# Kernel tuning notes

Measured on AMD Instinct MI355X. Metric: run time of the kernel, lower is better.

## Reference

```python
import math
import jax, jax.numpy as jnp
import numpy as np

B, S, D, H, FF = 2, 2048, 1024, 16, 4096
DH = D // H
NUM_BUCKETS, MAX_DISTANCE = 32, 128
EPS_LN = 1e-5


def setup_inputs() -> dict:
    key = jax.random.key(0)
    ks = jax.random.split(key, 12)
    sc = 0.02
    return {
        "x": jax.random.normal(ks[0], (B, S, D), dtype=jnp.float32),
        "Wq": jax.random.normal(ks[1], (D, D), dtype=jnp.float32) * sc,
        "bq": jnp.zeros((D,), jnp.float32),
        "Wk": jax.random.normal(ks[2], (D, D), dtype=jnp.float32) * sc,
        "bk": jnp.zeros((D,), jnp.float32),
        "Wv": jax.random.normal(ks[3], (D, D), dtype=jnp.float32) * sc,
        "bv": jnp.zeros((D,), jnp.float32),
        "Wo": jax.random.normal(ks[4], (D, D), dtype=jnp.float32) * sc,
        "bo": jnp.zeros((D,), jnp.float32),
        "W1": jax.random.normal(ks[5], (D, FF), dtype=jnp.float32) * sc,
        "b1": jnp.zeros((FF,), jnp.float32),
        "W2": jax.random.normal(ks[6], (FF, D), dtype=jnp.float32) * sc,
        "b2": jnp.zeros((D,), jnp.float32),
        "g1": jnp.ones((D,), jnp.float32),
        "beta1": jnp.zeros((D,), jnp.float32),
        "g2": jnp.ones((D,), jnp.float32),
        "beta2": jnp.zeros((D,), jnp.float32),
        "rel_emb": jax.random.normal(ks[7], (NUM_BUCKETS, H), dtype=jnp.float32) * sc,
        "pad_mask": jnp.ones((B, 1, 1, S), dtype=jnp.bool_),
    }


def _rel_bias(rel_emb, qlen, klen):
    # T5 bidirectional relative position bucketing; n = q_pos - k_pos
    q = jnp.arange(qlen)[:, None]
    k = jnp.arange(klen)[None, :]
    n = q - k
    half = NUM_BUCKETS // 2           # 16
    ret = (n < 0).astype(jnp.int32) * half
    n_abs = jnp.abs(n)
    max_exact = half // 2             # 8
    log_ratio = math.log(MAX_DISTANCE / max_exact)
    val_large = (max_exact + jnp.log(n_abs.astype(jnp.float32) / max_exact + 1e-6)
                 / log_ratio * (half - max_exact)).astype(jnp.int32)
    val_large = jnp.minimum(val_large, half - 1)
    bucket = jnp.where(n_abs < max_exact, n_abs.astype(jnp.int32), val_large) + ret
    bias = rel_emb[bucket]            # [Q, K, H]
    return jnp.transpose(bias, (2, 0, 1))[None]  # [1, H, Q, K]


def _layernorm(x, g, b):
    mu = jnp.mean(x, axis=-1, keepdims=True)
    var = jnp.mean(jnp.square(x - mu), axis=-1, keepdims=True)
    return (x - mu) * jax.lax.rsqrt(var + EPS_LN) * g + b


def reference(x, Wq, bq, Wk, bk, Wv, bv, Wo, bo, W1, b1, W2, b2,
              g1, beta1, g2, beta2, rel_emb, pad_mask):
    b_, s_, d_ = x.shape
    rel = _rel_bias(rel_emb, s_, s_)
    h = _layernorm(x, g1, beta1)
    q = (h @ Wq + bq).reshape(b_, s_, H, DH)
    k = (h @ Wk + bk).reshape(b_, s_, H, DH)
    v = (h @ Wv + bv).reshape(b_, s_, H, DH)
    scores = jnp.einsum("bqhd,bkhd->bhqk", q, k) / math.sqrt(DH)
    scores = scores + rel
    scores = jnp.where(pad_mask, scores, jnp.finfo(scores.dtype).min)
    attn = jax.nn.softmax(scores, axis=-1)
    out = jnp.einsum("bhqk,bkhd->bqhd", attn, v).reshape(b_, s_, d_)
    x = x + (out @ Wo + bo)
    h2 = _layernorm(x, g2, beta2)
    ff = jax.nn.gelu(h2 @ W1 + b1, approximate=False) @ W2 + b2
    return x + ff
```

## Files before the change

### kernel.cpp

```cpp
#include <hip/hip_runtime.h>
#include <hip/hip_bf16.h>
#include <math.h>

#define S_LEN 2048
#define DMODEL 1024
#define NHEAD 16
#define FFDIM 4096
#define NTOK 4096
#define QKV_LD 3072

typedef __attribute__((ext_vector_type(8))) short bf16x8;
typedef __attribute__((ext_vector_type(4))) float f32x4;

static __device__ __forceinline__ unsigned short f2bf_bits(float f) {
    union { __hip_bfloat16 b; unsigned short u; } cv;
    cv.b = __float2bfloat16(f);
    return cv.u;
}

__global__ __launch_bounds__(256) void transpose_bf16(
    const float* __restrict__ in, __hip_bfloat16* __restrict__ out, int R, int C)
{
    __shared__ float tile[32][33];
    const int c0 = blockIdx.x * 32, r0 = blockIdx.y * 32;
    const int tx = threadIdx.x & 31, ty = threadIdx.x >> 5;
#pragma unroll
    for (int i = 0; i < 4; i++) {
        int r = ty + i * 8;
        tile[r][tx] = in[(long)(r0 + r) * C + c0 + tx];
    }
    __syncthreads();
#pragma unroll
    for (int i = 0; i < 4; i++) {
        int c = ty + i * 8;
        out[(long)(c0 + c) * R + r0 + tx] = __float2bfloat16(tile[tx][c]);
    }
}

__global__ __launch_bounds__(256) void transpose_qkv_v(
    const __hip_bfloat16* __restrict__ in,
    __hip_bfloat16* __restrict__ out)
{
    __shared__ __hip_bfloat16 tile[32][33];
    const int bz = blockIdx.z;
    const int c0 = blockIdx.x * 32, r0 = blockIdx.y * 32;
    const int tx = threadIdx.x & 31, ty = threadIdx.x >> 5;
    const long ibase = (long)bz * S_LEN * QKV_LD;
#pragma unroll
    for (int i = 0; i < 4; i++) {
        int r = ty + i * 8;
        tile[r][tx] = in[ibase + (long)(r0 + r) * QKV_LD + c0 + tx];
    }
    __syncthreads();
    const long obase = (long)bz * DMODEL * S_LEN;
#pragma unroll
    for (int i = 0; i < 4; i++) {
        int c = ty + i * 8;
        out[obase + (long)(c0 + c) * S_LEN + r0 + tx] = tile[tx][c];
    }
}

__global__ __launch_bounds__(256) void biastab_kernel(
    const float* __restrict__ rel_emb, float* __restrict__ tab)
{
    int i = blockIdx.x * 256 + threadIdx.x;
    int h = i >> 12, idx = i & 4095;
    if (h >= NHEAD || idx >= 4095) return;
    int n = idx - 2047;
    int ret = (n < 0) ? 16 : 0;
    int na = (n < 0) ? -n : n;
    int bucket;
    if (na < 8) {
        bucket = na;
    } else {
        float vv = 8.0f + logf((float)na * 0.125f + 1e-6f) * (8.0f / 2.7725887222397811f);
        int vi = (int)vv;
        bucket = (vi < 15) ? vi : 15;
    }
    bucket += ret;
    tab[h * 4096 + idx] = rel_emb[bucket * NHEAD + h];
}

__global__ __launch_bounds__(256) void ln_bf16(
    const float* __restrict__ x, const float* __restrict__ gm,
    const float* __restrict__ bt, __hip_bfloat16* __restrict__ out)
{
    const long row = blockIdx.x;
    const int tid = threadIdx.x, w = tid >> 6;
    float4 v = ((const float4*)(x + row * DMODEL))[tid];
    float s = v.x + v.y + v.z + v.w;
#pragma unroll
    for (int m = 32; m >= 1; m >>= 1) s += __shfl_xor(s, m);
    __shared__ float red[4], red2[4];
    if ((tid & 63) == 0) red[w] = s;
    __syncthreads();
    float mu = (red[0] + red[1] + red[2] + red[3]) * (1.0f / DMODEL);
    float dx = v.x - mu, dy = v.y - mu, dz = v.z - mu, dw = v.w - mu;
    float s2 = dx * dx + dy * dy + dz * dz + dw * dw;
#pragma unroll
    for (int m = 32; m >= 1; m >>= 1) s2 += __shfl_xor(s2, m);
    if ((tid & 63) == 0) red2[w] = s2;
    __syncthreads();
    float var = (red2[0] + red2[1] + red2[2] + red2[3]) * (1.0f / DMODEL);
    float rs = rsqrtf(var + 1e-5f);
    float4 g4 = ((const float4*)gm)[tid];
    float4 b4 = ((const float4*)bt)[tid];
    long o = row * DMODEL + tid * 4;
    out[o + 0] = __float2bfloat16(dx * rs * g4.x + b4.x);
    out[o + 1] = __float2bfloat16(dy * rs * g4.y + b4.y);
    out[o + 2] = __float2bfloat16(dz * rs * g4.z + b4.z);
    out[o + 3] = __float2bfloat16(dw * rs * g4.w + b4.w);
}

template<int EPI>
__global__ __launch_bounds__(256) void gemm_bt(
    const __hip_bfloat16* __restrict__ A,
    const __hip_bfloat16* __restrict__ Bt,
    const float* __restrict__ bias,
    const float* __restrict__ bias2,
    const float* __restrict__ bias3,
    const float* __restrict__ resid,
    float* __restrict__ outf,
    __hip_bfloat16* __restrict__ outb,
    int K, int N)
{
    __shared__ __hip_bfloat16 As[128 * 32];
    __shared__ __hip_bfloat16 Bs[128 * 32];
    const int tid = threadIdx.x;
    const int lane = tid & 63, w = tid >> 6;
    const int cl = lane & 15, g = lane >> 4;
    const int wr = w >> 1, wc = w & 1;
    const int bm = blockIdx.x, bn = blockIdx.y;

    f32x4 acc[4][4] = {};

    const __hip_bfloat16* agp0 = A + (long)(bm * 128 + (tid >> 2)) * K + (tid & 3) * 8;
    const __hip_bfloat16* agp1 = agp0 + (long)64 * K;
    const __hip_bfloat16* bgp0 = Bt + (long)(bn * 128 + (tid >> 2)) * K + (tid & 3) * 8;
    const __hip_bfloat16* bgp1 = bgp0 + (long)64 * K;
    char* ldsA0 = (char*)As + w * 1024;
    char* ldsA1 = (char*)As + 4096 + w * 1024;
    char* ldsB0 = (char*)Bs + w * 1024;
    char* ldsB1 = (char*)Bs + 4096 + w * 1024;

    for (int k0 = 0; k0 < K; k0 += 32) {
        __syncthreads();
        __builtin_amdgcn_global_load_lds((const __attribute__((address_space(1))) void*)(agp0 + k0),
                                         (__attribute__((address_space(3))) void*)ldsA0, 16, 0, 0);
        __builtin_amdgcn_global_load_lds((const __attribute__((address_space(1))) void*)(agp1 + k0),
                                         (__attribute__((address_space(3))) void*)ldsA1, 16, 0, 0);
        __builtin_amdgcn_global_load_lds((const __attribute__((address_space(1))) void*)(bgp0 + k0),
                                         (__attribute__((address_space(3))) void*)ldsB0, 16, 0, 0);
        __builtin_amdgcn_global_load_lds((const __attribute__((address_space(1))) void*)(bgp1 + k0),
                                         (__attribute__((address_space(3))) void*)ldsB1, 16, 0, 0);
        __syncthreads();
        bf16x8 af[4], bfv[4];
#pragma unroll
        for (int m = 0; m < 4; m++)
            af[m] = *reinterpret_cast<const bf16x8*>(&As[(wr * 64 + m * 16 + cl) * 32 + g * 8]);
#pragma unroll
        for (int n = 0; n < 4; n++)
            bfv[n] = *reinterpret_cast<const bf16x8*>(&Bs[(wc * 64 + n * 16 + cl) * 32 + g * 8]);
#pragma unroll
        for (int m = 0; m < 4; m++)
#pragma unroll
            for (int n = 0; n < 4; n++)
                acc[m][n] = __builtin_amdgcn_mfma_f32_16x16x32_bf16(af[m], bfv[n], acc[m][n], 0, 0, 0);
    }

#pragma unroll
    for (int m = 0; m < 4; m++) {
#pragma unroll
        for (int n = 0; n < 4; n++) {
#pragma unroll
            for (int r = 0; r < 4; r++) {
                int row = bm * 128 + wr * 64 + m * 16 + g * 4 + r;
                int col = bn * 128 + wc * 64 + n * 16 + cl;
                long off = (long)row * N + col;
                if (EPI == 1) {
                    float vv = acc[m][n][r] + bias[col];
                    outf[off] = vv + resid[off];
                } else if (EPI == 2) {
                    float vv = acc[m][n][r] + bias[col];
                    float ge = 0.5f * vv * (1.0f + erff(vv * 0.70710678118654752f));
                    outb[off] = __float2bfloat16(ge);
                } else {
                    const float* bp = (col < 1024) ? bias : ((col < 2048) ? bias2 : bias3);
                    float vv = acc[m][n][r] + bp[col & 1023];
                    outb[off] = __float2bfloat16(vv);
                }
            }
        }
    }
}

__global__ __launch_bounds__(512, 4) void attn_fwd(
    const __hip_bfloat16* __restrict__ qkv,
    const __hip_bfloat16* __restrict__ vt,
    const float* __restrict__ btab,
    __hip_bfloat16* __restrict__ out)
{
    __shared__ __hip_bfloat16 Ks[2][64 * 64];
    __shared__ __hip_bfloat16 Vs[2][64 * 64];
    __shared__ __hip_bfloat16 Pl[8][16 * 64];
    const int tid = threadIdx.x, lane = tid & 63, w = tid >> 6;
    const int cl = lane & 15, g = lane >> 4;
    const int swz = (blockIdx.x & 7) * 64 + (blockIdx.x >> 3);
    const int bh = swz >> 4, qblk = swz & 15;
    const int b = bh >> 4, h = bh & 15;
    const int q0 = qblk * 128;
    const long qbase = ((long)b * S_LEN) * QKV_LD + h * 64;
    const __hip_bfloat16* vbase = vt + (long)b * DMODEL * S_LEN + (long)(h * 64) * S_LEN;

    const int srow = tid >> 3, scol = (tid & 7) ^ (srow & 7);
    const __hip_bfloat16* kstage = qkv + qbase + 1024 + (long)srow * QKV_LD + scol * 8;
    const __hip_bfloat16* vstage = vbase + (long)srow * S_LEN + scol * 8;

    const int qrow_a = q0 + w * 16 + cl;
    bf16x8 aq[2];
    aq[0] = *reinterpret_cast<const bf16x8*>(qkv + qbase + (long)qrow_a * QKV_LD + g * 8);
    aq[1] = *reinterpret_cast<const bf16x8*>(qkv + qbase + (long)qrow_a * QKV_LD + 32 + g * 8);

    f32x4 accO[4] = {};
    float mrun[4], lrun[4];
#pragma unroll
    for (int r = 0; r < 4; r++) { mrun[r] = -INFINITY; lrun[r] = 0.0f; }

    const int qrow_c = q0 + w * 16 + g * 4;

    auto STAGE = [&](int buf, int kv) {
        __builtin_amdgcn_global_load_lds(
            (const __attribute__((address_space(1))) void*)(kstage + (long)kv * QKV_LD),
            (__attribute__((address_space(3))) void*)((char*)&Ks[buf][0] + w * 1024), 16, 0, 0);
        __builtin_amdgcn_global_load_lds(
            (const __attribute__((address_space(1))) void*)(vstage + kv),
            (__attribute__((address_space(3))) void*)((char*)&Vs[buf][0] + w * 1024), 16, 0, 0);
    };

    STAGE(0, 0);
    __syncthreads();
    int cur = 0;

    for (int kv0 = 0; kv0 < S_LEN; kv0 += 64) {
        if (kv0 + 64 < S_LEN) STAGE(cur ^ 1, kv0 + 64);
        f32x4 accS[4] = {};
#pragma unroll
        for (int nf = 0; nf < 4; nf++) {
            int row = nf * 16 + cl;
#pragma unroll
            for (int ks2 = 0; ks2 < 2; ks2++) {
                int bo = row * 128 + ((((ks2 * 4 + g)) ^ (row & 7)) << 4);
                bf16x8 bk = *reinterpret_cast<const bf16x8*>((const char*)&Ks[cur][0] + bo);
                accS[nf] = __builtin_amdgcn_mfma_f32_16x16x32_bf16(aq[ks2], bk, accS[nf], 0, 0, 0);
            }
        }
        float sc[4][4], pmax[4];
#pragma unroll
        for (int r = 0; r < 4; r++) pmax[r] = -INFINITY;
#pragma unroll
        for (int nf = 0; nf < 4; nf++) {
            int col = kv0 + nf * 16 + cl;
#pragma unroll
            for (int r = 0; r < 4; r++) {
                int row = qrow_c + r;
                float s = accS[nf][r] * 0.125f + btab[h * 4096 + (row - col + 2047)];
                sc[nf][r] = s;
                pmax[r] = fmaxf(pmax[r], s);
            }
        }
#pragma unroll
        for (int r = 0; r < 4; r++) {
            pmax[r] = fmaxf(pmax[r], __shfl_xor(pmax[r], 1));
            pmax[r] = fmaxf(pmax[r], __shfl_xor(pmax[r], 2));
            pmax[r] = fmaxf(pmax[r], __shfl_xor(pmax[r], 4));
            pmax[r] = fmaxf(pmax[r], __shfl_xor(pmax[r], 8));
        }
        float mnew[4], alpha[4], psum[4];
#pragma unroll
        for (int r = 0; r < 4; r++) {
            mnew[r] = fmaxf(mrun[r], pmax[r]);
            alpha[r] = __expf(mrun[r] - mnew[r]);
            psum[r] = 0.0f;
        }
#pragma unroll
        for (int nf = 0; nf < 4; nf++) {
#pragma unroll
            for (int r = 0; r < 4; r++) {
                float p = __expf(sc[nf][r] - mnew[r]);
                psum[r] += p;
                int row_l = g * 4 + r, col_l = nf * 16 + cl;
                int bo = ((row_l * 64 + col_l) * 2) ^ ((row_l & 7) << 4);
                *reinterpret_cast<unsigned short*>(reinterpret_cast<char*>(&Pl[w][0]) + bo) = f2bf_bits(p);
            }
        }
#pragma unroll
        for (int r = 0; r < 4; r++) {
            psum[r] += __shfl_xor(psum[r], 1);
            psum[r] += __shfl_xor(psum[r], 2);
            psum[r] += __shfl_xor(psum[r], 4);
            psum[r] += __shfl_xor(psum[r], 8);
            lrun[r] = lrun[r] * alpha[r] + psum[r];
            mrun[r] = mnew[r];
#pragma unroll
            for (int df = 0; df < 4; df++) accO[df][r] *= alpha[r];
        }
        asm volatile("s_waitcnt lgkmcnt(0)" ::: "memory");
        __builtin_amdgcn_sched_barrier(0);
#pragma unroll
        for (int ks2 = 0; ks2 < 2; ks2++) {
            int bo = ((cl * 64 + ks2 * 32 + g * 8) * 2) ^ ((cl & 7) << 4);
            bf16x8 ap = *reinterpret_cast<const bf16x8*>(reinterpret_cast<const char*>(&Pl[w][0]) + bo);
#pragma unroll
            for (int df = 0; df < 4; df++) {
                int row = df * 16 + cl;
                int bo2 = row * 128 + ((((ks2 * 4 + g)) ^ (row & 7)) << 4);
                bf16x8 bv = *reinterpret_cast<const bf16x8*>((const char*)&Vs[cur][0] + bo2);
                accO[df] = __builtin_amdgcn_mfma_f32_16x16x32_bf16(ap, bv, accO[df], 0, 0, 0);
            }
        }
        __syncthreads();
        cur ^= 1;
    }
#pragma unroll
    for (int df = 0; df < 4; df++) {
#pragma unroll
        for (int r = 0; r < 4; r++) {
            int row = qrow_c + r;
            int col = df * 16 + cl;
            out[((long)b * S_LEN + row) * DMODEL + h * 64 + col] = __float2bfloat16(accO[df][r] / lrun[r]);
        }
    }
}

extern "C" void kernel_launch(void* const* d_in, const int* in_sizes, int n_in,
                              void* d_out, int out_size, void* d_ws, size_t ws_size,
                              hipStream_t stream) {
    (void)in_sizes; (void)n_in; (void)out_size; (void)ws_size;
    const float* x   = (const float*)d_in[0];
    const float* Wq  = (const float*)d_in[1];
    const float* bq  = (const float*)d_in[2];
    const float* Wk  = (const float*)d_in[3];
    const float* bk  = (const float*)d_in[4];
    const float* Wv  = (const float*)d_in[5];
    const float* bv  = (const float*)d_in[6];
    const float* Wo  = (const float*)d_in[7];
    const float* bo  = (const float*)d_in[8];
    const float* W1  = (const float*)d_in[9];
    const float* b1  = (const float*)d_in[10];
    const float* W2  = (const float*)d_in[11];
    const float* b2  = (const float*)d_in[12];
    const float* g1  = (const float*)d_in[13];
    const float* be1 = (const float*)d_in[14];
    const float* g2  = (const float*)d_in[15];
    const float* be2 = (const float*)d_in[16];
    const float* rel = (const float*)d_in[17];
    float* outp = (float*)d_out;

    char* ws = (char*)d_ws;
    __hip_bfloat16* Wqkvt = (__hip_bfloat16*)(ws + ((size_t)0  << 20));
    __hip_bfloat16* Wot   = (__hip_bfloat16*)(ws + ((size_t)6  << 20));
    __hip_bfloat16* W1t   = (__hip_bfloat16*)(ws + ((size_t)8  << 20));
    __hip_bfloat16* W2t   = (__hip_bfloat16*)(ws + ((size_t)16 << 20));
    __hip_bfloat16* hb    = (__hip_bfloat16*)(ws + ((size_t)24 << 20));
    __hip_bfloat16* qkvb  = (__hip_bfloat16*)(ws + ((size_t)32 << 20));
    __hip_bfloat16* vtb   = (__hip_bfloat16*)(ws + ((size_t)56 << 20));
    __hip_bfloat16* ao    = (__hip_bfloat16*)(ws + ((size_t)64 << 20));
    float*          x2    = (float*)         (ws + ((size_t)72 << 20));
    __hip_bfloat16* h2b   = (__hip_bfloat16*)(ws + ((size_t)88 << 20));
    __hip_bfloat16* ffb   = (__hip_bfloat16*)(ws + ((size_t)24 << 20));
    float*          btb   = (float*)         (ws + ((size_t)96 << 20));

    dim3 blk(256);
    transpose_bf16<<<dim3(32, 32),  blk, 0, stream>>>(Wq, Wqkvt,                1024, 1024);
    transpose_bf16<<<dim3(32, 32),  blk, 0, stream>>>(Wk, Wqkvt + 1024 * 1024,  1024, 1024);
    transpose_bf16<<<dim3(32, 32),  blk, 0, stream>>>(Wv, Wqkvt + 2048 * 1024,  1024, 1024);
    transpose_bf16<<<dim3(32, 32),  blk, 0, stream>>>(Wo, Wot, 1024, 1024);
    transpose_bf16<<<dim3(128, 32), blk, 0, stream>>>(W1, W1t, 1024, 4096);
    transpose_bf16<<<dim3(32, 128), blk, 0, stream>>>(W2, W2t, 4096, 1024);
    biastab_kernel<<<dim3(256), blk, 0, stream>>>(rel, btb);
    ln_bf16<<<dim3(NTOK), blk, 0, stream>>>(x, g1, be1, hb);
    gemm_bt<3><<<dim3(32, 24), blk, 0, stream>>>(hb, Wqkvt, bq, bk, bv, nullptr, nullptr, qkvb, 1024, 3072);
    transpose_qkv_v<<<dim3(32, 64, 2), blk, 0, stream>>>(qkvb + 2048, vtb);
    attn_fwd<<<dim3(512), dim3(512), 0, stream>>>(qkvb, vtb, btb, ao);
    gemm_bt<1><<<dim3(32, 8), blk, 0, stream>>>(ao, Wot, bo, nullptr, nullptr, x, x2, nullptr, 1024, 1024);
    ln_bf16<<<dim3(NTOK), blk, 0, stream>>>(x2, g2, be2, h2b);
    gemm_bt<2><<<dim3(32, 32), blk, 0, stream>>>(h2b, W1t, b1, nullptr, nullptr, nullptr, nullptr, ffb, 1024, 4096);
    gemm_bt<1><<<dim3(32, 8), blk, 0, stream>>>(ffb, W2t, b2, nullptr, nullptr, x2, outp, nullptr, 4096, 1024);
}
```

Baseline: 483.9 us.

## Add 256x256 pipelined GEMM for QKV/FFN1 and double-buffer the 128-tile GEMM

```diff
diff --git a/kernel.cpp b/kernel.cpp
--- a/kernel.cpp
+++ b/kernel.cpp
@@ -17,6 +17,10 @@
     cv.b = __float2bfloat16(f);
     return cv.u;
 }
+
+#define GLOAD16(src, dst) \
+    __builtin_amdgcn_global_load_lds((const __attribute__((address_space(1))) void*)(src), \
+                                     (__attribute__((address_space(3))) void*)(dst), 16, 0, 0)
 
 __global__ __launch_bounds__(256) void transpose_bf16(
     const float* __restrict__ in, __hip_bfloat16* __restrict__ out, int R, int C)
@@ -117,15 +121,13 @@
     const __hip_bfloat16* __restrict__ A,
     const __hip_bfloat16* __restrict__ Bt,
     const float* __restrict__ bias,
-    const float* __restrict__ bias2,
-    const float* __restrict__ bias3,
     const float* __restrict__ resid,
     float* __restrict__ outf,
     __hip_bfloat16* __restrict__ outb,
     int K, int N)
 {
-    __shared__ __hip_bfloat16 As[128 * 32];
-    __shared__ __hip_bfloat16 Bs[128 * 32];
+    __shared__ __hip_bfloat16 As[2][128 * 32];
+    __shared__ __hip_bfloat16 Bs[2][128 * 32];
     const int tid = threadIdx.x;
     const int lane = tid & 63, w = tid >> 6;
     const int cl = lane & 15, g = lane >> 4;
@@ -138,34 +140,38 @@
     const __hip_bfloat16* agp1 = agp0 + (long)64 * K;
     const __hip_bfloat16* bgp0 = Bt + (long)(bn * 128 + (tid >> 2)) * K + (tid & 3) * 8;
     const __hip_bfloat16* bgp1 = bgp0 + (long)64 * K;
-    char* ldsA0 = (char*)As + w * 1024;
-    char* ldsA1 = (char*)As + 4096 + w * 1024;
-    char* ldsB0 = (char*)Bs + w * 1024;
-    char* ldsB1 = (char*)Bs + 4096 + w * 1024;
-
+
+    auto STAGE = [&](int buf, int k0) {
+        GLOAD16(agp0 + k0, (char*)&As[buf][0] + w * 1024);
+        GLOAD16(agp1 + k0, (char*)&As[buf][0] + 4096 + w * 1024);
+        GLOAD16(bgp0 + k0, (char*)&Bs[buf][0] + w * 1024);
+        GLOAD16(bgp1 + k0, (char*)&Bs[buf][0] + 4096 + w * 1024);
+    };
+
+    STAGE(0, 0);
+    asm volatile("s_waitcnt vmcnt(0)" ::: "memory");
+    __builtin_amdgcn_s_barrier();
+
+    int cur = 0;
     for (int k0 = 0; k0 < K; k0 += 32) {
-        __syncthreads();
-        __builtin_amdgcn_global_load_lds((const __attribute__((address_space(1))) void*)(agp0 + k0),
-                                         (__attribute__((address_space(3))) void*)ldsA0, 16, 0, 0);
-        __builtin_amdgcn_global_load_lds((const __attribute__((address_space(1))) void*)(agp1 + k0),
-                                         (__attribute__((address_space(3))) void*)ldsA1, 16, 0, 0);
-        __builtin_amdgcn_global_load_lds((const __attribute__((address_space(1))) void*)(bgp0 + k0),
-                                         (__attribute__((address_space(3))) void*)ldsB0, 16, 0, 0);
-        __builtin_amdgcn_global_load_lds((const __attribute__((address_space(1))) void*)(bgp1 + k0),
-                                         (__attribute__((address_space(3))) void*)ldsB1, 16, 0, 0);
-        __syncthreads();
+        if (k0 + 32 < K) STAGE(cur ^ 1, k0 + 32);
         bf16x8 af[4], bfv[4];
 #pragma unroll
         for (int m = 0; m < 4; m++)
-            af[m] = *reinterpret_cast<const bf16x8*>(&As[(wr * 64 + m * 16 + cl) * 32 + g * 8]);
+            af[m] = *reinterpret_cast<const bf16x8*>(&As[cur][(wr * 64 + m * 16 + cl) * 32 + g * 8]);
 #pragma unroll
         for (int n = 0; n < 4; n++)
-            bfv[n] = *reinterpret_cast<const bf16x8*>(&Bs[(wc * 64 + n * 16 + cl) * 32 + g * 8]);
+            bfv[n] = *reinterpret_cast<const bf16x8*>(&Bs[cur][(wc * 64 + n * 16 + cl) * 32 + g * 8]);
+        __builtin_amdgcn_s_setprio(1);
 #pragma unroll
         for (int m = 0; m < 4; m++)
 #pragma unroll
             for (int n = 0; n < 4; n++)
                 acc[m][n] = __builtin_amdgcn_mfma_f32_16x16x32_bf16(af[m], bfv[n], acc[m][n], 0, 0, 0);
+        __builtin_amdgcn_s_setprio(0);
+        asm volatile("s_waitcnt vmcnt(0)" ::: "memory");
+        __builtin_amdgcn_s_barrier();
+        cur ^= 1;
     }
 
 #pragma unroll
@@ -176,11 +182,131 @@
             for (int r = 0; r < 4; r++) {
                 int row = bm * 128 + wr * 64 + m * 16 + g * 4 + r;
                 int col = bn * 128 + wc * 64 + n * 16 + cl;
+                float vv = acc[m][n][r] + bias[col];
                 long off = (long)row * N + col;
                 if (EPI == 1) {
-                    float vv = acc[m][n][r] + bias[col];
                     outf[off] = vv + resid[off];
-                } else if (EPI == 2) {
+                } else {
+                    outb[off] = __float2bfloat16(vv);
+                }
+            }
+        }
+    }
+}
+
+template<int EPI>
+__global__ __launch_bounds__(512, 2) void gemm256(
+    const __hip_bfloat16* __restrict__ A,
+    const __hip_bfloat16* __restrict__ Bt,
+    const float* __restrict__ bias,
+    const float* __restrict__ bias2,
+    const float* __restrict__ bias3,
+    __hip_bfloat16* __restrict__ outb,
+    int K, int N)
+{
+    __shared__ char L[131072];
+    const int tid = threadIdx.x, lane = tid & 63, w = tid >> 6;
+    const int cl = lane & 15, g = lane >> 4;
+    const int wm = w >> 2, wn = w & 3;
+    const int nbn = N >> 8;
+    const int nwg = 16 * nbn;
+    const int bid = blockIdx.x;
+    const int swz = (bid & 7) * (nwg >> 3) + (bid >> 3);
+    const int bm = swz / nbn, bn = swz - bm * nbn;
+    const int NT = K >> 6;
+
+    f32x4 acc[8][4] = {};
+
+    const int srow = tid >> 3;
+    const int scol = ((tid & 7) ^ (srow & 7)) * 8;
+    const __hip_bfloat16* Asrc = A  + (long)(bm * 256 + srow) * K + scol;
+    const __hip_bfloat16* Bsrc = Bt + (long)(bn * 256 + srow) * K + scol;
+
+    auto STAGE_A = [&](int buf, int half, int t) {
+        const __hip_bfloat16* s = Asrc + (long)(half * 128) * K + t * 64;
+        char* d = L + buf * 32768 + half * 16384 + w * 1024;
+        GLOAD16(s, d);
+        GLOAD16(s + (long)64 * K, d + 8192);
+    };
+    auto STAGE_B = [&](int buf, int half, int t) {
+        const __hip_bfloat16* s = Bsrc + (long)(half * 128) * K + t * 64;
+        char* d = L + 65536 + buf * 32768 + half * 16384 + w * 1024;
+        GLOAD16(s, d);
+        GLOAD16(s + (long)64 * K, d + 8192);
+    };
+
+    const char* arb = L + wm * 16384 + cl * 128;
+    const char* brb = L + 65536 + (wn >> 1) * 16384 + (((wn & 1) * 64 + cl)) * 128;
+    const int xo0 = (g * 16) ^ ((cl & 7) << 4);
+    const int xo1 = (64 + g * 16) ^ ((cl & 7) << 4);
+
+    STAGE_B(0, 0, 0); STAGE_B(0, 1, 0);
+    STAGE_A(0, 0, 0); STAGE_A(0, 1, 0);
+    STAGE_B(1, 0, 1); STAGE_B(1, 1, 1);
+    asm volatile("s_waitcnt vmcnt(4)" ::: "memory");
+    __builtin_amdgcn_s_barrier();
+
+    bf16x8 bfr[4][2];
+    for (int t2 = 0; t2 < NT; t2 += 2) {
+        const bool more = (t2 + 2 < NT);
+#pragma unroll
+        for (int p = 0; p < 8; p++) {
+            const int buf = p >> 2, mp = p & 3;
+            const int bo = buf * 32768;
+            if (mp == 0) {
+#pragma unroll
+                for (int n = 0; n < 4; n++) {
+                    bfr[n][0] = *reinterpret_cast<const bf16x8*>(brb + bo + n * 2048 + xo0);
+                    bfr[n][1] = *reinterpret_cast<const bf16x8*>(brb + bo + n * 2048 + xo1);
+                }
+            }
+            bf16x8 a0k0 = *reinterpret_cast<const bf16x8*>(arb + bo + (mp * 2) * 2048 + xo0);
+            bf16x8 a0k1 = *reinterpret_cast<const bf16x8*>(arb + bo + (mp * 2) * 2048 + xo1);
+            bf16x8 a1k0 = *reinterpret_cast<const bf16x8*>(arb + bo + (mp * 2 + 1) * 2048 + xo0);
+            bf16x8 a1k1 = *reinterpret_cast<const bf16x8*>(arb + bo + (mp * 2 + 1) * 2048 + xo1);
+            if (p == 0)      { STAGE_A(1, 0, t2 + 1); }
+            else if (p == 1) { STAGE_A(1, 1, t2 + 1); }
+            else if (p == 2) { if (more) STAGE_B(0, 0, t2 + 2); }
+            else if (p == 3) { if (more) STAGE_B(0, 1, t2 + 2); }
+            else if (p == 4) { if (more) STAGE_A(0, 0, t2 + 2); }
+            else if (p == 5) { if (more) STAGE_A(0, 1, t2 + 2); }
+            else if (p == 6) { if (more) STAGE_B(1, 0, t2 + 3); }
+            else             { if (more) STAGE_B(1, 1, t2 + 3); }
+            __builtin_amdgcn_s_barrier();
+            __builtin_amdgcn_s_setprio(1);
+#pragma unroll
+            for (int i = 0; i < 2; i++) {
+                const int ma = mp * 2 + i;
+                bf16x8 ak0 = i ? a1k0 : a0k0;
+                bf16x8 ak1 = i ? a1k1 : a0k1;
+#pragma unroll
+                for (int n = 0; n < 4; n++) {
+                    acc[ma][n] = __builtin_amdgcn_mfma_f32_16x16x32_bf16(ak0, bfr[n][0], acc[ma][n], 0, 0, 0);
+                    acc[ma][n] = __builtin_amdgcn_mfma_f32_16x16x32_bf16(ak1, bfr[n][1], acc[ma][n], 0, 0, 0);
+                }
+            }
+            __builtin_amdgcn_s_setprio(0);
+            if (p == 3) {
+                if (more) { asm volatile("s_waitcnt vmcnt(4)" ::: "memory"); }
+                else      { asm volatile("s_waitcnt vmcnt(0)" ::: "memory"); }
+            }
+            if (p == 7) {
+                if (more) { asm volatile("s_waitcnt vmcnt(4)" ::: "memory"); }
+            }
+            __builtin_amdgcn_s_barrier();
+        }
+    }
+
+#pragma unroll
+    for (int m = 0; m < 8; m++) {
+#pragma unroll
+        for (int n = 0; n < 4; n++) {
+#pragma unroll
+            for (int r = 0; r < 4; r++) {
+                int row = bm * 256 + wm * 128 + m * 16 + g * 4 + r;
+                int col = bn * 256 + wn * 64 + n * 16 + cl;
+                long off = (long)row * N + col;
+                if (EPI == 2) {
                     float vv = acc[m][n][r] + bias[col];
                     float ge = 0.5f * vv * (1.0f + erff(vv * 0.70710678118654752f));
                     outb[off] = __float2bfloat16(ge);
@@ -229,12 +355,8 @@
     const int qrow_c = q0 + w * 16 + g * 4;
 
     auto STAGE = [&](int buf, int kv) {
-        __builtin_amdgcn_global_load_lds(
-            (const __attribute__((address_space(1))) void*)(kstage + (long)kv * QKV_LD),
-            (__attribute__((address_space(3))) void*)((char*)&Ks[buf][0] + w * 1024), 16, 0, 0);
-        __builtin_amdgcn_global_load_lds(
-            (const __attribute__((address_space(1))) void*)(vstage + kv),
-            (__attribute__((address_space(3))) void*)((char*)&Vs[buf][0] + w * 1024), 16, 0, 0);
+        GLOAD16(kstage + (long)kv * QKV_LD, (char*)&Ks[buf][0] + w * 1024);
+        GLOAD16(vstage + kv, (char*)&Vs[buf][0] + w * 1024);
     };
 
     STAGE(0, 0);
@@ -379,11 +501,11 @@
     transpose_bf16<<<dim3(32, 128), blk, 0, stream>>>(W2, W2t, 4096, 1024);
     biastab_kernel<<<dim3(256), blk, 0, stream>>>(rel, btb);
     ln_bf16<<<dim3(NTOK), blk, 0, stream>>>(x, g1, be1, hb);
-    gemm_bt<3><<<dim3(32, 24), blk, 0, stream>>>(hb, Wqkvt, bq, bk, bv, nullptr, nullptr, qkvb, 1024, 3072);
+    gemm256<3><<<dim3(192), dim3(512), 0, stream>>>(hb, Wqkvt, bq, bk, bv, qkvb, 1024, 3072);
     transpose_qkv_v<<<dim3(32, 64, 2), blk, 0, stream>>>(qkvb + 2048, vtb);
     attn_fwd<<<dim3(512), dim3(512), 0, stream>>>(qkvb, vtb, btb, ao);
-    gemm_bt<1><<<dim3(32, 8), blk, 0, stream>>>(ao, Wot, bo, nullptr, nullptr, x, x2, nullptr, 1024, 1024);
+    gemm_bt<1><<<dim3(32, 8), blk, 0, stream>>>(ao, Wot, bo, x, x2, nullptr, 1024, 1024);
     ln_bf16<<<dim3(NTOK), blk, 0, stream>>>(x2, g2, be2, h2b);
-    gemm_bt<2><<<dim3(32, 32), blk, 0, stream>>>(h2b, W1t, b1, nullptr, nullptr, nullptr, nullptr, ffb, 1024, 4096);
-    gemm_bt<1><<<dim3(32, 8), blk, 0, stream>>>(ffb, W2t, b2, nullptr, nullptr, x2, outp, nullptr, 4096, 1024);
-}
+    gemm256<2><<<dim3(256), dim3(512), 0, stream>>>(h2b, W1t, b1, nullptr, nullptr, ffb, 1024, 4096);
+    gemm_bt<1><<<dim3(32, 8), blk, 0, stream>>>(ffb, W2t, b2, x2, outp, nullptr, 4096, 1024);
+}
```

New measurement: 456.5 us. 1.06x faster.
